# Kernel tuning notes

Measured on AMD Instinct MI355X. Metric: run time of the kernel, lower is better.

Reference implementation:

```python
import jax, jax.numpy as jnp
import numpy as np

SUPPORT_TH = 0.5 ** 2   # supporth_th ** 2
MAX_ITER = 10
FEATURE_NORM = True


def setup_inputs() -> dict:
    key = jax.random.key(0)
    k1, k2, k3, k4 = jax.random.split(key, 4)
    B, C, N = 2, 256, 4096
    return {
        "pcloud1": jax.random.uniform(k1, (B, 3, N), dtype=jnp.float32),
        "pcloud2": jax.random.uniform(k2, (B, 3, N), dtype=jnp.float32),
        "feats1": jax.random.normal(k3, (B, C, N), dtype=jnp.float32),
        "feats2": jax.random.normal(k4, (B, C, N), dtype=jnp.float32),
        "gamma": jnp.zeros((1,), dtype=jnp.float32),
        "epsilon": jnp.zeros((1,), dtype=jnp.float32),
    }


def _sinkhorn(K, epsilon, gamma, max_iter):
    # K: [B, N1, N2] affinity; entropic-regularized OT with relaxed marginals
    B, N1, N2 = K.shape
    power = gamma / (gamma + epsilon)          # scalar (shape [1])
    prob1 = jnp.full((B, N1, 1), 1.0 / N1, K.dtype)
    prob2 = jnp.full((B, N2, 1), 1.0 / N2, K.dtype)
    a0 = prob1

    def body(ab, _):
        a, _ = ab
        KTa = jnp.matmul(K.transpose(0, 2, 1), a)           # [B, N2, 1]
        b = (prob2 / (KTa + 1e-8)) ** power
        Kb = jnp.matmul(K, b)                               # [B, N1, 1]
        a = (prob1 / (Kb + 1e-8)) ** power
        return (a, b), None

    (a, b), _ = jax.lax.scan(body, (a0, prob2), None, length=max_iter)
    # Transport plan T = diag(a) K diag(b)
    return a * K * b.transpose(0, 2, 1)


def reference(pcloud1, pcloud2, feats1, feats2, gamma, epsilon):
    # pcloud*: [B, 3, N]; feats*: [B, C, N] -> flow_init: [B, N, 3]
    p1 = pcloud1.transpose(0, 2, 1)   # [B, N, 3]
    p2 = pcloud2.transpose(0, 2, 1)
    f1 = feats1.transpose(0, 2, 1)    # [B, N, C]
    f2 = feats2.transpose(0, 2, 1)
    eps = jnp.exp(epsilon) + 0.03                # shape [1]
    gam = jnp.exp(gamma) + 0.03                  # shape [1]

    if FEATURE_NORM:
        f1 = f1 / jnp.sqrt(jnp.sum(f1 ** 2, -1, keepdims=True) + 1e-6)
        f2 = f2 / jnp.sqrt(jnp.sum(f2 ** 2, -1, keepdims=True) + 1e-6)
        corr = jnp.einsum('bnc,bmc->bnm', f1, f2)
    else:
        corr = jnp.einsum('bnc,bmc->bnm', f1, f2) / (f1.shape[2] ** 0.5)

    # pairwise squared distances: [B, N1, N2]
    dist = (jnp.sum(p1 ** 2, -1, keepdims=True)
            + jnp.sum(p2 ** 2, -1, keepdims=True).transpose(0, 2, 1)
            - 2.0 * jnp.einsum('bnc,bmc->bnm', p1, p2))
    support = (dist < SUPPORT_TH).astype(corr.dtype)

    K = jnp.exp(-(1.0 - corr) / eps) * support   # affinity kernel
    T = _sinkhorn(K, eps, gam, MAX_ITER)

    row_sum = jnp.sum(T, -1, keepdims=True)
    flow_init = jnp.matmul(T, p2) / (row_sum + 1e-6) - p1   # [B, N, 3]
    return flow_init
```

## Files before the change

### kernel.cpp

```cpp
#include <hip/hip_runtime.h>
#include <hip/hip_fp16.h>
#include <math.h>

#define NB 2
#define NC 256
#define NN 4096
#define MAX_ITER 10

#define PBLOCKS 512
#define PCHUNKS 256
#define PROWS 16

#define LDA 72
#define C8S 144

typedef _Float16 half8_t __attribute__((ext_vector_type(8)));
typedef float f32x4 __attribute__((ext_vector_type(4)));
typedef float f32x2 __attribute__((ext_vector_type(2)));

__device__ inline void fp8x16_decode(uint4 v, float* o) {
  f32x2 p;
  p = __builtin_amdgcn_cvt_pk_f32_fp8(v.x, false); o[0] = p[0];  o[1] = p[1];
  p = __builtin_amdgcn_cvt_pk_f32_fp8(v.x, true);  o[2] = p[0];  o[3] = p[1];
  p = __builtin_amdgcn_cvt_pk_f32_fp8(v.y, false); o[4] = p[0];  o[5] = p[1];
  p = __builtin_amdgcn_cvt_pk_f32_fp8(v.y, true);  o[6] = p[0];  o[7] = p[1];
  p = __builtin_amdgcn_cvt_pk_f32_fp8(v.z, false); o[8] = p[0];  o[9] = p[1];
  p = __builtin_amdgcn_cvt_pk_f32_fp8(v.z, true);  o[10] = p[0]; o[11] = p[1];
  p = __builtin_amdgcn_cvt_pk_f32_fp8(v.w, false); o[12] = p[0]; o[13] = p[1];
  p = __builtin_amdgcn_cvt_pk_f32_fp8(v.w, true);  o[14] = p[0]; o[15] = p[1];
}

__global__ __launch_bounds__(256) void norms_kernel(
    const float* __restrict__ f1, const float* __restrict__ f2,
    float* __restrict__ inv1, float* __restrict__ inv2) {
  int n = blockIdx.x * 256 + threadIdx.x;
  int b = blockIdx.y;
  const float* f = blockIdx.z ? f2 : f1;
  float* o = blockIdx.z ? inv2 : inv1;
  const float* base = f + (size_t)b * NC * NN + n;
  float s = 0.f;
#pragma unroll 8
  for (int c = 0; c < NC; ++c) {
    float v = base[(size_t)c * NN];
    s = fmaf(v, v, s);
  }
  o[b * NN + n] = 1.0f / sqrtf(s + 1e-6f);
}

__global__ __launch_bounds__(256) void prep_kernel(
    const float* __restrict__ f1, const float* __restrict__ f2,
    const float* __restrict__ inv1, const float* __restrict__ inv2,
    __half* __restrict__ f1t, __half* __restrict__ f2t) {
  int which = blockIdx.z & 1;
  int b = blockIdx.z >> 1;
  const float* f = which ? f2 : f1;
  const float* inv = which ? inv2 : inv1;
  __half* ft = which ? f2t : f1t;
  int n0 = blockIdx.x * 64;
  int c0 = blockIdx.y * 64;

  __shared__ float T[64][65];
  int t = threadIdx.x;
  int lane = t & 63, grp = t >> 6;
#pragma unroll
  for (int p = 0; p < 16; ++p) {
    int c_in = p * 4 + grp;
    T[lane][c_in] = f[((size_t)b * NC + c0 + c_in) * NN + n0 + lane];
  }
  __syncthreads();
#pragma unroll
  for (int p = 0; p < 16; ++p) {
    int n_out = p * 4 + grp;
    float v = T[n_out][lane] * inv[b * NN + n0 + n_out];
    ft[((size_t)b * NN + n0 + n_out) * NC + c0 + lane] = __float2half(v);
  }
}

struct __align__(16) SMstage { __half A[128 * LDA]; __half B[128 * LDA]; };
union SMu { SMstage st; unsigned char C8[128 * C8S]; };

__global__ __launch_bounds__(256) void kmat_mfma_kernel(
    const __half* __restrict__ f1t, const __half* __restrict__ f2t,
    const float* __restrict__ pc1, const float* __restrict__ pc2,
    const float* __restrict__ g_eps, unsigned char* __restrict__ K) {
  int b = blockIdx.z;
  int i0 = blockIdx.y * 128;
  int j0 = blockIdx.x * 128;

  __shared__ SMu sm;
  __shared__ float p1s[4][128];
  __shared__ float p2s[4][128];

  int tid = threadIdx.x;
  if (tid < 128) {
    int i = i0 + tid;
    float x = pc1[((size_t)b * 3 + 0) * NN + i];
    float y = pc1[((size_t)b * 3 + 1) * NN + i];
    float z = pc1[((size_t)b * 3 + 2) * NN + i];
    p1s[0][tid] = x; p1s[1][tid] = y; p1s[2][tid] = z;
    p1s[3][tid] = x * x + y * y + z * z;
  } else {
    int j = j0 + tid - 128;
    float x = pc2[((size_t)b * 3 + 0) * NN + j];
    float y = pc2[((size_t)b * 3 + 1) * NN + j];
    float z = pc2[((size_t)b * 3 + 2) * NN + j];
    p2s[0][tid - 128] = x; p2s[1][tid - 128] = y; p2s[2][tid - 128] = z;
    p2s[3][tid - 128] = x * x + y * y + z * z;
  }
  float inv_eps = 1.0f / (expf(g_eps[0]) + 0.03f);

  const __half* Ag = f1t + ((size_t)b * NN + i0) * NC;
  const __half* Bg = f2t + ((size_t)b * NN + j0) * NC;

  int lane = tid & 63, wid = tid >> 6;
  int m0 = (wid >> 1) * 64, n0 = (wid & 1) * 64;
  int l15 = lane & 15, quad = lane >> 4;

  f32x4 acc[4][4] = {};

  int sr = tid >> 1, sh = tid & 1;

  for (int kk = 0; kk < NC; kk += 64) {
    __syncthreads();
    {
      const uint4* As = (const uint4*)(Ag + (size_t)sr * NC + kk + sh * 32);
      const uint4* Bs = (const uint4*)(Bg + (size_t)sr * NC + kk + sh * 32);
      uint4* Ad = (uint4*)&sm.st.A[sr * LDA + sh * 32];
      uint4* Bd = (uint4*)&sm.st.B[sr * LDA + sh * 32];
#pragma unroll
      for (int s = 0; s < 4; ++s) Ad[s] = As[s];
#pragma unroll
      for (int s = 0; s < 4; ++s) Bd[s] = Bs[s];
    }
    __syncthreads();
#pragma unroll
    for (int ks = 0; ks < 2; ++ks) {
      half8_t aF[4], bF[4];
#pragma unroll
      for (int mt = 0; mt < 4; ++mt)
        aF[mt] = *(const half8_t*)&sm.st.A[(m0 + mt * 16 + l15) * LDA + ks * 32 + quad * 8];
#pragma unroll
      for (int nt = 0; nt < 4; ++nt)
        bF[nt] = *(const half8_t*)&sm.st.B[(n0 + nt * 16 + l15) * LDA + ks * 32 + quad * 8];
#pragma unroll
      for (int mt = 0; mt < 4; ++mt)
#pragma unroll
        for (int nt = 0; nt < 4; ++nt)
          acc[mt][nt] = __builtin_amdgcn_mfma_f32_16x16x32_f16(
              aF[mt], bF[nt], acc[mt][nt], 0, 0, 0);
    }
  }

  __syncthreads();

  float c2x[4], c2y[4], c2z[4], c2n[4];
#pragma unroll
  for (int nt = 0; nt < 4; ++nt) {
    int c = n0 + nt * 16 + l15;
    c2x[nt] = p2s[0][c]; c2y[nt] = p2s[1][c];
    c2z[nt] = p2s[2][c]; c2n[nt] = p2s[3][c];
  }
#pragma unroll
  for (int mt = 0; mt < 4; ++mt) {
#pragma unroll
    for (int rr = 0; rr < 4; ++rr) {
      int row = m0 + mt * 16 + quad * 4 + rr;
      float px = p1s[0][row], py = p1s[1][row], pz = p1s[2][row];
      float n1 = p1s[3][row];
#pragma unroll
      for (int nt = 0; nt < 4; ++nt) {
        float corr = acc[mt][nt][rr];
        float dist = n1 + c2n[nt] - 2.0f * (px * c2x[nt] + py * c2y[nt] + pz * c2z[nt]);
        float kv = (dist < 0.25f) ? __expf((corr - 1.0f) * inv_eps) : 0.0f;
        unsigned int pk = (unsigned int)__builtin_amdgcn_cvt_pk_fp8_f32(kv, kv, 0, false);
        sm.C8[row * C8S + n0 + nt * 16 + l15] = (unsigned char)(pk & 0xFF);
      }
    }
  }
  __syncthreads();

  int c8 = tid & 7, rg = tid >> 3;
#pragma unroll
  for (int s = 0; s < 4; ++s) {
    int row = s * 32 + rg;
    uint4 v = *(uint4*)&sm.C8[row * C8S + c8 * 16];
    *(uint4*)&K[((size_t)b * NN + i0 + row) * NN + j0 + c8 * 16] = v;
  }
}

__global__ __launch_bounds__(256) void fused_pass_kernel(
    const unsigned char* __restrict__ K, const float* __restrict__ bvec,
    float* __restrict__ part, const float* __restrict__ g_gamma,
    const float* __restrict__ g_eps, int pass) {
  __shared__ float wgt_s[PROWS];

  int g = blockIdx.x;
  int batch = g >> 8;
  int row0 = (g & 255) * PROWS;
  int tid = threadIdx.x;
  int w = tid >> 6, l = tid & 63;
  const unsigned char* Kb = K + (size_t)batch * NN * NN;

  float eps = expf(g_eps[0]) + 0.03f;
  float gam = expf(g_gamma[0]) + 0.03f;
  float power = gam / (gam + eps);
  const float probN = 1.0f / NN;

  if (pass > 0) {
    int rbase = row0 + w * 4;

    float breg[64];
#pragma unroll
    for (int q = 0; q < 4; ++q) {
      const float4* bp = (const float4*)&bvec[batch * NN + (q * 64 + l) * 16];
#pragma unroll
      for (int s = 0; s < 4; ++s) {
        float4 bb = bp[s];
        breg[q * 16 + s * 4 + 0] = bb.x;
        breg[q * 16 + s * 4 + 1] = bb.y;
        breg[q * 16 + s * 4 + 2] = bb.z;
        breg[q * 16 + s * 4 + 3] = bb.w;
      }
    }

    uint4 kraw[4][4];
#pragma unroll
    for (int r = 0; r < 4; ++r) {
      const uint4* Kr = (const uint4*)(Kb + (size_t)(rbase + r) * NN);
#pragma unroll
      for (int q = 0; q < 4; ++q) kraw[r][q] = Kr[q * 64 + l];
    }

#pragma unroll
    for (int r = 0; r < 4; ++r) {
      float a0 = 0.f, a1 = 0.f, a2 = 0.f, a3 = 0.f;
#pragma unroll
      for (int q = 0; q < 4; ++q) {
        float kf[16];
        fp8x16_decode(kraw[r][q], kf);
#pragma unroll
        for (int s = 0; s < 4; ++s) {
          a0 = fmaf(kf[s * 4 + 0], breg[q * 16 + s * 4 + 0], a0);
          a1 = fmaf(kf[s * 4 + 1], breg[q * 16 + s * 4 + 1], a1);
          a2 = fmaf(kf[s * 4 + 2], breg[q * 16 + s * 4 + 2], a2);
          a3 = fmaf(kf[s * 4 + 3], breg[q * 16 + s * 4 + 3], a3);
        }
      }
      float kbs = (a0 + a1) + (a2 + a3);
#pragma unroll
      for (int off = 1; off < 64; off <<= 1) kbs += __shfl_xor(kbs, off, 64);
      if (l == 0) wgt_s[w * 4 + r] = __powf(probN / (kbs + 1e-8f), power);
    }
  }

  __builtin_amdgcn_sched_barrier(0);

  uint4 k2[16];
#pragma unroll
  for (int r = 0; r < PROWS; ++r)
    k2[r] = *(const uint4*)(Kb + (size_t)(row0 + r) * NN + w * 1024 + l * 16);

  if (pass > 0) __syncthreads();

  float ps[16];
#pragma unroll
  for (int e = 0; e < 16; ++e) ps[e] = 0.f;
#pragma unroll
  for (int r = 0; r < PROWS; ++r) {
    float wr = (pass == 0) ? probN : wgt_s[r];
    float kf[16];
    fp8x16_decode(k2[r], kf);
#pragma unroll
    for (int e = 0; e < 16; ++e) ps[e] = fmaf(kf[e], wr, ps[e]);
  }

  float* pout = &part[(size_t)g * NN + w * 1024 + l * 16];
#pragma unroll
  for (int s = 0; s < 4; ++s)
    *(float4*)&pout[s * 4] = make_float4(ps[s * 4 + 0], ps[s * 4 + 1],
                                         ps[s * 4 + 2], ps[s * 4 + 3]);
}

__global__ __launch_bounds__(256) void breduce_kernel(
    const float* __restrict__ part, float* __restrict__ bvec,
    const float* __restrict__ g_gamma, const float* __restrict__ g_eps) {
  int b = blockIdx.y;
  int c0 = blockIdx.x * 64;
  int t = threadIdx.x;
  int cl = t & 63, kg = t >> 6;
  const float* p = part + (size_t)(b * PCHUNKS + kg * 64) * NN + c0 + cl;
  float s = 0.f;
#pragma unroll 8
  for (int k = 0; k < 64; ++k) s += p[(size_t)k * NN];
  __shared__ float red[4][64];
  red[kg][cl] = s;
  __syncthreads();
  if (t < 64) {
    float tot = (red[0][t] + red[1][t]) + (red[2][t] + red[3][t]);
    float eps = expf(g_eps[0]) + 0.03f;
    float gam = expf(g_gamma[0]) + 0.03f;
    float power = gam / (gam + eps);
    bvec[b * NN + c0 + t] = __powf((1.0f / NN) / (tot + 1e-8f), power);
  }
}

__global__ __launch_bounds__(256) void kb_flow_kernel(
    const unsigned char* __restrict__ K, const float* __restrict__ bvec,
    const float* __restrict__ pc1, const float* __restrict__ pc2,
    const float* __restrict__ g_gamma, const float* __restrict__ g_eps,
    float* __restrict__ out) {
  int b = blockIdx.y;
  int i = blockIdx.x;
  int j16 = threadIdx.x;
  const uint4* K16 = (const uint4*)(K + ((size_t)b * NN + i) * NN);
  uint4 kv = K16[j16];
  float kf[16];
  fp8x16_decode(kv, kf);

  const float4* b4 = (const float4*)&bvec[b * NN + j16 * 16];
  const float* p2 = pc2 + (size_t)b * 3 * NN;
  const float4* p2x = (const float4*)&p2[0 * NN + j16 * 16];
  const float4* p2y = (const float4*)&p2[1 * NN + j16 * 16];
  const float4* p2z = (const float4*)&p2[2 * NN + j16 * 16];

  float S = 0.f, Sx = 0.f, Sy = 0.f, Sz = 0.f;
#pragma unroll
  for (int s = 0; s < 4; ++s) {
    float4 bb = b4[s];
    float4 xx = p2x[s], yy = p2y[s], zz = p2z[s];
    float w0 = kf[s * 4 + 0] * bb.x;
    float w1 = kf[s * 4 + 1] * bb.y;
    float w2 = kf[s * 4 + 2] * bb.z;
    float w3 = kf[s * 4 + 3] * bb.w;
    S += (w0 + w1) + (w2 + w3);
    Sx += w0 * xx.x + w1 * xx.y + w2 * xx.z + w3 * xx.w;
    Sy += w0 * yy.x + w1 * yy.y + w2 * yy.z + w3 * yy.w;
    Sz += w0 * zz.x + w1 * zz.y + w2 * zz.z + w3 * zz.w;
  }
#pragma unroll
  for (int off = 32; off; off >>= 1) {
    S  += __shfl_down(S, off, 64);
    Sx += __shfl_down(Sx, off, 64);
    Sy += __shfl_down(Sy, off, 64);
    Sz += __shfl_down(Sz, off, 64);
  }
  __shared__ float red[4][4];
  int lane = threadIdx.x & 63, wid = threadIdx.x >> 6;
  if (lane == 0) {
    red[wid][0] = S; red[wid][1] = Sx; red[wid][2] = Sy; red[wid][3] = Sz;
  }
  __syncthreads();
  if (threadIdx.x == 0) {
    float kb  = red[0][0] + red[1][0] + red[2][0] + red[3][0];
    float Sxt = red[0][1] + red[1][1] + red[2][1] + red[3][1];
    float Syt = red[0][2] + red[1][2] + red[2][2] + red[3][2];
    float Szt = red[0][3] + red[1][3] + red[2][3] + red[3][3];
    float eps = expf(g_eps[0]) + 0.03f;
    float gam = expf(g_gamma[0]) + 0.03f;
    float power = gam / (gam + eps);
    float av = powf((1.0f / NN) / (kb + 1e-8f), power);
    float denom = av * kb + 1e-6f;
    const float* p1 = pc1 + (size_t)b * 3 * NN;
    size_t o = ((size_t)b * NN + i) * 3;
    out[o + 0] = av * Sxt / denom - p1[0 * NN + i];
    out[o + 1] = av * Syt / denom - p1[1 * NN + i];
    out[o + 2] = av * Szt / denom - p1[2 * NN + i];
  }
}

extern "C" void kernel_launch(void* const* d_in, const int* in_sizes, int n_in,
                              void* d_out, int out_size, void* d_ws,
                              size_t ws_size, hipStream_t stream) {
  const float* pc1 = (const float*)d_in[0];
  const float* pc2 = (const float*)d_in[1];
  const float* f1 = (const float*)d_in[2];
  const float* f2 = (const float*)d_in[3];
  const float* g_gamma = (const float*)d_in[4];
  const float* g_eps = (const float*)d_in[5];
  float* out = (float*)d_out;

  size_t off = 0;
  char* ws = (char*)d_ws;
  unsigned char* K = (unsigned char*)(ws + off);
  off += (size_t)NB * NN * NN * sizeof(unsigned char);
  __half* f1t = (__half*)(ws + off); off += (size_t)NB * NN * NC * sizeof(__half);
  __half* f2t = (__half*)(ws + off); off += (size_t)NB * NN * NC * sizeof(__half);
  float* inv1 = (float*)(ws + off); off += (size_t)NB * NN * sizeof(float);
  float* inv2 = (float*)(ws + off); off += (size_t)NB * NN * sizeof(float);
  float* bvec = (float*)(ws + off); off += (size_t)NB * NN * sizeof(float);
  float* part = (float*)(ws + off); off += (size_t)PBLOCKS * NN * sizeof(float);
  if (ws_size < off) return;

  norms_kernel<<<dim3(NN / 256, NB, 2), 256, 0, stream>>>(f1, f2, inv1, inv2);
  prep_kernel<<<dim3(NN / 64, NC / 64, NB * 2), 256, 0, stream>>>(
      f1, f2, inv1, inv2, f1t, f2t);
  kmat_mfma_kernel<<<dim3(NN / 128, NN / 128, NB), 256, 0, stream>>>(
      f1t, f2t, pc1, pc2, g_eps, K);

  for (int it = 0; it < MAX_ITER; ++it) {
    fused_pass_kernel<<<dim3(PBLOCKS), 256, 0, stream>>>(
        K, bvec, part, g_gamma, g_eps, it);
    breduce_kernel<<<dim3(NN / 64, NB), 256, 0, stream>>>(
        part, bvec, g_gamma, g_eps);
  }

  kb_flow_kernel<<<dim3(NN, NB), 256, 0, stream>>>(K, bvec, pc1, pc2,
                                                   g_gamma, g_eps, out);
}
```

Before: 350.6 us.

## Double 512-thread fused pass and register-prefetch K-tile loads in MFMA kernel

The fused Sinkhorn pass kernel now launches 512 threads per block. Each of the 8 waves handles 2 rows for the Kb dot product and 8 bytes per lane for the column pass. This lowers the per-thread register footprint (no 64-float breg array, smaller k2) so more memory loads can be in flight. Separately, the MFMA K-matrix kernel prefetches the next 64-wide k-slice from global memory into registers while the current slice is computed, overlapping load latency with MFMA work. The risks are more shuffle reductions per block, narrower per-thread loads, and added register pressure in the GEMM.

```diff
diff --git a/kernel.cpp b/kernel.cpp
--- a/kernel.cpp
+++ b/kernel.cpp
@@ -28,6 +28,14 @@
   p = __builtin_amdgcn_cvt_pk_f32_fp8(v.z, true);  o[10] = p[0]; o[11] = p[1];
   p = __builtin_amdgcn_cvt_pk_f32_fp8(v.w, false); o[12] = p[0]; o[13] = p[1];
   p = __builtin_amdgcn_cvt_pk_f32_fp8(v.w, true);  o[14] = p[0]; o[15] = p[1];
+}
+
+__device__ inline void fp8x8_decode(uint2 v, float* o) {
+  f32x2 p;
+  p = __builtin_amdgcn_cvt_pk_f32_fp8(v.x, false); o[0] = p[0]; o[1] = p[1];
+  p = __builtin_amdgcn_cvt_pk_f32_fp8(v.x, true);  o[2] = p[0]; o[3] = p[1];
+  p = __builtin_amdgcn_cvt_pk_f32_fp8(v.y, false); o[4] = p[0]; o[5] = p[1];
+  p = __builtin_amdgcn_cvt_pk_f32_fp8(v.y, true);  o[6] = p[0]; o[7] = p[1];
 }
 
 __global__ __launch_bounds__(256) void norms_kernel(
@@ -119,20 +127,34 @@
   f32x4 acc[4][4] = {};
 
   int sr = tid >> 1, sh = tid & 1;
-
-  for (int kk = 0; kk < NC; kk += 64) {
+  const __half* Arow = Ag + (size_t)sr * NC + sh * 32;
+  const __half* Brow = Bg + (size_t)sr * NC + sh * 32;
+
+  uint4 rA[4], rB[4];
+#pragma unroll
+  for (int s = 0; s < 4; ++s) {
+    rA[s] = ((const uint4*)Arow)[s];
+    rB[s] = ((const uint4*)Brow)[s];
+  }
+
+  for (int t = 0; t < 4; ++t) {
     __syncthreads();
     {
-      const uint4* As = (const uint4*)(Ag + (size_t)sr * NC + kk + sh * 32);
-      const uint4* Bs = (const uint4*)(Bg + (size_t)sr * NC + kk + sh * 32);
       uint4* Ad = (uint4*)&sm.st.A[sr * LDA + sh * 32];
       uint4* Bd = (uint4*)&sm.st.B[sr * LDA + sh * 32];
 #pragma unroll
-      for (int s = 0; s < 4; ++s) Ad[s] = As[s];
-#pragma unroll
-      for (int s = 0; s < 4; ++s) Bd[s] = Bs[s];
+      for (int s = 0; s < 4; ++s) Ad[s] = rA[s];
+#pragma unroll
+      for (int s = 0; s < 4; ++s) Bd[s] = rB[s];
     }
     __syncthreads();
+    if (t < 3) {
+#pragma unroll
+      for (int s = 0; s < 4; ++s) {
+        rA[s] = ((const uint4*)(Arow + (t + 1) * 64))[s];
+        rB[s] = ((const uint4*)(Brow + (t + 1) * 64))[s];
+      }
+    }
 #pragma unroll
     for (int ks = 0; ks < 2; ++ks) {
       half8_t aF[4], bF[4];
@@ -188,7 +210,7 @@
   }
 }
 
-__global__ __launch_bounds__(256) void fused_pass_kernel(
+__global__ __launch_bounds__(512) void fused_pass_kernel(
     const unsigned char* __restrict__ K, const float* __restrict__ bvec,
     float* __restrict__ part, const float* __restrict__ g_gamma,
     const float* __restrict__ g_eps, int pass) {
@@ -207,78 +229,73 @@
   const float probN = 1.0f / NN;
 
   if (pass > 0) {
-    int rbase = row0 + w * 4;
-
-    float breg[64];
+    int rbase = row0 + w * 2;
+
+    uint4 kraw[2][4];
+#pragma unroll
+    for (int r = 0; r < 2; ++r) {
+      const uint4* Kr = (const uint4*)(Kb + (size_t)(rbase + r) * NN);
+#pragma unroll
+      for (int q = 0; q < 4; ++q) kraw[r][q] = Kr[q * 64 + l];
+    }
+
+    float d0[2] = {}, d1[2] = {}, d2[2] = {}, d3[2] = {};
 #pragma unroll
     for (int q = 0; q < 4; ++q) {
+      float bq[16];
       const float4* bp = (const float4*)&bvec[batch * NN + (q * 64 + l) * 16];
 #pragma unroll
       for (int s = 0; s < 4; ++s) {
         float4 bb = bp[s];
-        breg[q * 16 + s * 4 + 0] = bb.x;
-        breg[q * 16 + s * 4 + 1] = bb.y;
-        breg[q * 16 + s * 4 + 2] = bb.z;
-        breg[q * 16 + s * 4 + 3] = bb.w;
+        bq[s * 4 + 0] = bb.x; bq[s * 4 + 1] = bb.y;
+        bq[s * 4 + 2] = bb.z; bq[s * 4 + 3] = bb.w;
       }
-    }
-
-    uint4 kraw[4][4];
-#pragma unroll
-    for (int r = 0; r < 4; ++r) {
-      const uint4* Kr = (const uint4*)(Kb + (size_t)(rbase + r) * NN);
-#pragma unroll
-      for (int q = 0; q < 4; ++q) kraw[r][q] = Kr[q * 64 + l];
-    }
-
-#pragma unroll
-    for (int r = 0; r < 4; ++r) {
-      float a0 = 0.f, a1 = 0.f, a2 = 0.f, a3 = 0.f;
-#pragma unroll
-      for (int q = 0; q < 4; ++q) {
+#pragma unroll
+      for (int r = 0; r < 2; ++r) {
         float kf[16];
         fp8x16_decode(kraw[r][q], kf);
 #pragma unroll
         for (int s = 0; s < 4; ++s) {
-          a0 = fmaf(kf[s * 4 + 0], breg[q * 16 + s * 4 + 0], a0);
-          a1 = fmaf(kf[s * 4 + 1], breg[q * 16 + s * 4 + 1], a1);
-          a2 = fmaf(kf[s * 4 + 2], breg[q * 16 + s * 4 + 2], a2);
-          a3 = fmaf(kf[s * 4 + 3], breg[q * 16 + s * 4 + 3], a3);
+          d0[r] = fmaf(kf[s * 4 + 0], bq[s * 4 + 0], d0[r]);
+          d1[r] = fmaf(kf[s * 4 + 1], bq[s * 4 + 1], d1[r]);
+          d2[r] = fmaf(kf[s * 4 + 2], bq[s * 4 + 2], d2[r]);
+          d3[r] = fmaf(kf[s * 4 + 3], bq[s * 4 + 3], d3[r]);
         }
       }
-      float kbs = (a0 + a1) + (a2 + a3);
+    }
+#pragma unroll
+    for (int r = 0; r < 2; ++r) {
+      float kbs = (d0[r] + d1[r]) + (d2[r] + d3[r]);
 #pragma unroll
       for (int off = 1; off < 64; off <<= 1) kbs += __shfl_xor(kbs, off, 64);
-      if (l == 0) wgt_s[w * 4 + r] = __powf(probN / (kbs + 1e-8f), power);
+      if (l == 0) wgt_s[w * 2 + r] = __powf(probN / (kbs + 1e-8f), power);
     }
   }
 
   __builtin_amdgcn_sched_barrier(0);
 
-  uint4 k2[16];
+  uint2 k2[PROWS];
 #pragma unroll
   for (int r = 0; r < PROWS; ++r)
-    k2[r] = *(const uint4*)(Kb + (size_t)(row0 + r) * NN + w * 1024 + l * 16);
+    k2[r] = *(const uint2*)(Kb + (size_t)(row0 + r) * NN + w * 512 + l * 8);
 
   if (pass > 0) __syncthreads();
 
-  float ps[16];
-#pragma unroll
-  for (int e = 0; e < 16; ++e) ps[e] = 0.f;
+  float ps[8];
+#pragma unroll
+  for (int e = 0; e < 8; ++e) ps[e] = 0.f;
 #pragma unroll
   for (int r = 0; r < PROWS; ++r) {
     float wr = (pass == 0) ? probN : wgt_s[r];
-    float kf[16];
-    fp8x16_decode(k2[r], kf);
-#pragma unroll
-    for (int e = 0; e < 16; ++e) ps[e] = fmaf(kf[e], wr, ps[e]);
-  }
-
-  float* pout = &part[(size_t)g * NN + w * 1024 + l * 16];
-#pragma unroll
-  for (int s = 0; s < 4; ++s)
-    *(float4*)&pout[s * 4] = make_float4(ps[s * 4 + 0], ps[s * 4 + 1],
-                                         ps[s * 4 + 2], ps[s * 4 + 3]);
+    float kf[8];
+    fp8x8_decode(k2[r], kf);
+#pragma unroll
+    for (int e = 0; e < 8; ++e) ps[e] = fmaf(kf[e], wr, ps[e]);
+  }
+
+  float* pout = &part[(size_t)g * NN + w * 512 + l * 8];
+  *(float4*)&pout[0] = make_float4(ps[0], ps[1], ps[2], ps[3]);
+  *(float4*)&pout[4] = make_float4(ps[4], ps[5], ps[6], ps[7]);
 }
 
 __global__ __launch_bounds__(256) void breduce_kernel(
@@ -398,7 +415,7 @@
       f1t, f2t, pc1, pc2, g_eps, K);
 
   for (int it = 0; it < MAX_ITER; ++it) {
-    fused_pass_kernel<<<dim3(PBLOCKS), 256, 0, stream>>>(
+    fused_pass_kernel<<<dim3(PBLOCKS), 512, 0, stream>>>(
         K, bvec, part, g_gamma, g_eps, it);
     breduce_kernel<<<dim3(NN / 64, NB), 256, 0, stream>>>(
         part, bvec, g_gamma, g_eps);
```

Result: slower. 402.7 us (+14.9%).
